# Kernel tuning notes

Hardware: AMD Instinct MI355X
Metric: run time of the kernel (lower is better)

## Reference

```python
import jax, jax.numpy as jnp
import numpy as np

N_GRAPHS = 8
NODES_PER_G = 1024
EDGES_PER_G = 2048
N = N_GRAPHS * NODES_PER_G          # 8192 nodes
E = N_GRAPHS * EDGES_PER_G          # 16384 edges
IN_DIM, EDGE_DIM, HID, OUT_DIM, T = 10, 9, 64, 3, 5
EPS = 1e-6


def _lin(key, fan_in, fan_out):
    kw, kb = jax.random.split(key)
    s = 1.0 / np.sqrt(fan_in)
    return (jax.random.uniform(kw, (fan_in, fan_out), jnp.float32, -s, s),
            jax.random.uniform(kb, (fan_out,), jnp.float32, -s, s))


def setup_inputs() -> dict:
    key = jax.random.key(0)
    ks = jax.random.split(key, 32)
    x = jax.random.normal(ks[0], (N, IN_DIM), jnp.float32)
    edge_attr = jax.random.normal(ks[1], (E, EDGE_DIM), jnp.float32)
    # edges stay within their own graph (block structure)
    src_l = jax.random.randint(ks[2], (E,), 0, NODES_PER_G)
    dst_l = jax.random.randint(ks[3], (E,), 0, NODES_PER_G)
    off = jnp.repeat(jnp.arange(N_GRAPHS, dtype=jnp.int64) * NODES_PER_G, EDGES_PER_G)
    edge_index = jnp.stack([src_l.astype(jnp.int64) + off, dst_l.astype(jnp.int64) + off])
    batch = jnp.repeat(jnp.arange(N_GRAPHS, dtype=jnp.int64), NODES_PER_G)

    lift_w1, lift_b1 = _lin(ks[4], IN_DIM, HID)
    lift_w2, lift_b2 = _lin(ks[5], HID, HID)
    proj_w1, proj_b1 = _lin(ks[6], HID, HID)
    proj_w2, proj_b2 = _lin(ks[7], HID, OUT_DIM)

    def stackp(fn, base):
        ws, bs = zip(*[fn(ks[base + t]) for t in range(T)])
        return jnp.stack(ws), jnp.stack(bs)

    root_w, root_b = stackp(lambda k: _lin(k, HID, HID), 8)
    k_w1, k_b1 = stackp(lambda k: _lin(k, EDGE_DIM, HID), 13)
    k_w2, k_b2 = stackp(lambda k: _lin(k, HID, HID), 18)
    k_w3, k_b3 = stackp(lambda k: _lin(k, HID, HID * HID), 23)

    return dict(x=x, edge_attr=edge_attr,
                lift_w1=lift_w1, lift_b1=lift_b1, lift_w2=lift_w2, lift_b2=lift_b2,
                root_w=root_w, root_b=root_b,
                k_w1=k_w1, k_b1=k_b1, k_w2=k_w2, k_b2=k_b2, k_w3=k_w3, k_b3=k_b3,
                proj_w1=proj_w1, proj_b1=proj_b1, proj_w2=proj_w2, proj_b2=proj_b2,
                edge_index=edge_index, batch=batch)


def reference(x, edge_attr, lift_w1, lift_b1, lift_w2, lift_b2,
              root_w, root_b, k_w1, k_b1, k_w2, k_b2, k_w3, k_b3,
              proj_w1, proj_b1, proj_w2, proj_b2, edge_index, batch):
    src, dst = edge_index[0], edge_index[1]

    # --- per-graph edge_attr standardization (scatter mean/std over each graph's edges) ---
    eb = batch[src]                                           # graph id per edge [E]
    ones_e = jnp.ones((E,), jnp.float32)
    cnt = jax.ops.segment_sum(ones_e, eb, num_segments=N_GRAPHS)          # [G]
    mean = jax.ops.segment_sum(edge_attr, eb, num_segments=N_GRAPHS) / cnt[:, None]
    msq = jax.ops.segment_sum(edge_attr * edge_attr, eb, num_segments=N_GRAPHS) / cnt[:, None]
    std = jnp.sqrt(jnp.clip(msq - mean * mean, 0.0))
    ea = (edge_attr - mean[eb]) / (std[eb] + EPS)             # [E, edge_dim]

    # --- lift MLP ---
    v = jax.nn.relu(x @ lift_w1 + lift_b1) @ lift_w2 + lift_b2  # [N, HID]

    # --- T kernel layers: v' = relu(W_root v + mean_{j->i} K(e_ij) v_j) ---
    deg = jnp.clip(jax.ops.segment_sum(ones_e, dst, num_segments=N), 1.0)  # [N]
    for t in range(T):
        h = jax.nn.relu(ea @ k_w1[t] + k_b1[t])
        h = jax.nn.relu(h @ k_w2[t] + k_b2[t])
        ker = (h @ k_w3[t] + k_b3[t]).reshape(E, HID, HID)    # per-edge 64x64 kernel
        msg = jnp.einsum('eij,ej->ei', ker, v[src])           # [E, HID]
        aggr = jax.ops.segment_sum(msg, dst, num_segments=N) / deg[:, None]
        v = jax.nn.relu(v @ root_w[t] + root_b[t] + aggr)
        # dropout (p=0.1) is identity in eval mode

    # --- project MLP ---
    return jax.nn.relu(v @ proj_w1 + proj_b1) @ proj_w2 + proj_b2  # [N, OUT_DIM]
```

## Files before the change

kernel.cpp:

```cpp
#include <hip/hip_runtime.h>

#define N_GRAPHS    8
#define EDGES_PER_G 2048
#define NN          8192
#define EE          16384
#define IN_DIM      10
#define EDGE_DIM    9
#define HID         64
#define OUT_DIM     3
#define TT          5
#define EPSN        1e-6f

typedef float f32x4 __attribute__((ext_vector_type(4)));
typedef short bf16x8s __attribute__((ext_vector_type(8)));

union BF8 { __bf16 h[8]; bf16x8s v; };

__device__ inline void gl_lds16(const unsigned short* g, unsigned short* l) {
  __builtin_amdgcn_global_load_lds(
      (const __attribute__((address_space(1))) unsigned int*)g,
      (__attribute__((address_space(3))) unsigned int*)l, 16, 0, 0);
}

__device__ inline void edgemlp16(int e0, int tid,
    const float* __restrict__ ear, const float* __restrict__ meanb,
    const float* __restrict__ invstd,
    const float* __restrict__ w1, const float* __restrict__ b1,
    const float* __restrict__ w2, const float* __restrict__ b2,
    float* smem, float* __restrict__ h2T) {
  float (*sh)[68] = (float (*)[68])smem;
  float (*st)[68] = (float (*)[68])(smem + 16 * 68);
  int g = tid >> 6, lane = tid & 63;
  int eb = e0 + g * 4;
  int gg = e0 >> 11;
  const float* mb = meanb + gg * EDGE_DIM;
  const float* is = invstd + gg * EDGE_DIM;
  float xn[4][EDGE_DIM];
#pragma unroll
  for (int k = 0; k < 4; ++k) {
    const float* er = ear + (size_t)(eb + k) * EDGE_DIM;
#pragma unroll
    for (int d = 0; d < EDGE_DIM; ++d) xn[k][d] = (er[d] - mb[d]) * is[d];
  }
  float a0 = b1[lane], a1 = a0, a2 = a0, a3 = a0;
#pragma unroll
  for (int d = 0; d < EDGE_DIM; ++d) {
    float w = w1[d * HID + lane];
    a0 += xn[0][d] * w; a1 += xn[1][d] * w;
    a2 += xn[2][d] * w; a3 += xn[3][d] * w;
  }
  sh[g * 4 + 0][lane] = fmaxf(a0, 0.f);
  sh[g * 4 + 1][lane] = fmaxf(a1, 0.f);
  sh[g * 4 + 2][lane] = fmaxf(a2, 0.f);
  sh[g * 4 + 3][lane] = fmaxf(a3, 0.f);
  __syncthreads();
  float o0 = b2[lane], o1 = o0, o2 = o0, o3 = o0;
#pragma unroll
  for (int h = 0; h < HID; ++h) {
    float w = w2[h * HID + lane];
    o0 += sh[g * 4 + 0][h] * w; o1 += sh[g * 4 + 1][h] * w;
    o2 += sh[g * 4 + 2][h] * w; o3 += sh[g * 4 + 3][h] * w;
  }
  st[g * 4 + 0][lane] = fmaxf(o0, 0.f);
  st[g * 4 + 1][lane] = fmaxf(o1, 0.f);
  st[g * 4 + 2][lane] = fmaxf(o2, 0.f);
  st[g * 4 + 3][lane] = fmaxf(o3, 0.f);
  __syncthreads();
  for (int i = tid; i < HID * 16; i += 256) {
    int c = i >> 4, eo = i & 15;
    h2T[(size_t)c * EE + e0 + eo] = st[eo][c];
  }
}

__global__ __launch_bounds__(256) void k_stats(
    const float* __restrict__ ear, float* __restrict__ meanb,
    float* __restrict__ invstd, float* __restrict__ degf) {
  __shared__ float sw[4][2 * EDGE_DIM];
  int b = blockIdx.x;
  int g = threadIdx.x >> 6, lane = threadIdx.x & 63;
  if (b < N_GRAPHS) {
    int gg = b;
    float ls[EDGE_DIM], lq[EDGE_DIM];
#pragma unroll
    for (int d = 0; d < EDGE_DIM; ++d) { ls[d] = 0.f; lq[d] = 0.f; }
    for (int e = threadIdx.x; e < EDGES_PER_G; e += blockDim.x) {
      const float* row = ear + (size_t)(gg * EDGES_PER_G + e) * EDGE_DIM;
#pragma unroll
      for (int d = 0; d < EDGE_DIM; ++d) { float xv = row[d]; ls[d] += xv; lq[d] += xv * xv; }
    }
#pragma unroll
    for (int d = 0; d < EDGE_DIM; ++d) {
#pragma unroll
      for (int off = 32; off > 0; off >>= 1) {
        ls[d] += __shfl_down(ls[d], off);
        lq[d] += __shfl_down(lq[d], off);
      }
    }
    if (lane == 0) {
#pragma unroll
      for (int d = 0; d < EDGE_DIM; ++d) {
        sw[g][d] = ls[d];
        sw[g][EDGE_DIM + d] = lq[d];
      }
    }
    __syncthreads();
    if (threadIdx.x < EDGE_DIM) {
      int d = threadIdx.x;
      float s0 = sw[0][d] + sw[1][d] + sw[2][d] + sw[3][d];
      float q0 = sw[0][EDGE_DIM + d] + sw[1][EDGE_DIM + d] +
                 sw[2][EDGE_DIM + d] + sw[3][EDGE_DIM + d];
      float m  = s0 * (1.0f / EDGES_PER_G);
      float mq = q0 * (1.0f / EDGES_PER_G);
      float var = fmaxf(mq - m * m, 0.f);
      meanb[gg * EDGE_DIM + d]  = m;
      invstd[gg * EDGE_DIM + d] = 1.f / (sqrtf(var) + EPSN);
    }
  } else {
    int idx = (b - N_GRAPHS) * 256 + threadIdx.x;
    ((float4*)degf)[idx] = make_float4(0.f, 0.f, 0.f, 0.f);
  }
}

#define PRE_EM0   (EE / 16)
#define PRE_LIFT  (NN / 4)
#define PRE_BPREP 1024
#define PRE_DEG   (EE / 256)
#define PRE_ZAG   (NN * HID / 1024)
__global__ __launch_bounds__(256) void k_pre(
    const float* __restrict__ x,
    const float* __restrict__ lw1, const float* __restrict__ lb1,
    const float* __restrict__ lw2, const float* __restrict__ lb2,
    float* __restrict__ v,
    const float* __restrict__ kw3, const float* __restrict__ kb3,
    unsigned short* __restrict__ Bbf,
    const int* __restrict__ dst, float* __restrict__ degf,
    const float* __restrict__ ear, const float* __restrict__ meanb,
    const float* __restrict__ invstd, float* __restrict__ aggr,
    const float* __restrict__ w1, const float* __restrict__ b1,
    const float* __restrict__ w2, const float* __restrict__ b2,
    float* __restrict__ h2T0) {
  __shared__ float smem[2 * 16 * 68];
  int b = blockIdx.x;
  int g = threadIdx.x >> 6, lane = threadIdx.x & 63;
  if (b < PRE_EM0) {
    edgemlp16(b * 16, threadIdx.x, ear, meanb, invstd, w1, b1, w2, b2,
              smem, h2T0);
  } else if (b < PRE_EM0 + PRE_LIFT) {
    float (*sh)[HID] = (float (*)[HID])smem;
    int n = (b - PRE_EM0) * 4 + g;
    const float* xr = x + n * IN_DIM;
    float a = lb1[lane];
#pragma unroll
    for (int d = 0; d < IN_DIM; ++d) a += xr[d] * lw1[d * HID + lane];
    sh[g][lane] = fmaxf(a, 0.f);
    __syncthreads();
    float o = lb2[lane];
#pragma unroll
    for (int h = 0; h < HID; ++h) o += sh[g][h] * lw2[h * HID + lane];
    v[n * HID + lane] = o;
  } else if (b < PRE_EM0 + PRE_LIFT + PRE_BPREP) {
    const int total = TT * 65 * 4096;
    for (int i = (b - (PRE_EM0 + PRE_LIFT)) * 256 + (int)threadIdx.x; i < total;
         i += PRE_BPREP * 256) {
      int xx   = i & 4095;
      int call = i >> 12;
      int t = call / 65;
      int c = call - t * 65;
      int sn = xx >> 9;
      int s  = sn >> 2, nt = sn & 3;
      int l9 = xx & 511;
      int ln = l9 >> 3, jj = l9 & 7;
      int nn15 = ln & 15, qq = ln >> 4;
      int x_in = (nt * 16 + nn15) * 64 + s * 32 + qq * 8 + jj;
      float val = (c < 64) ? kw3[(size_t)(t * 64 + c) * 4096 + x_in]
                           : kb3[(size_t)t * 4096 + x_in];
      union { __bf16 h; unsigned short s16; } u;
      u.h = (__bf16)val;
      Bbf[i] = u.s16;
    }
  } else if (b < PRE_EM0 + PRE_LIFT + PRE_BPREP + PRE_DEG) {
    int e = (b - (PRE_EM0 + PRE_LIFT + PRE_BPREP)) * 256 + threadIdx.x;
    atomicAdd(&degf[dst[e]], 1.f);
  } else {
    int idx = (b - (PRE_EM0 + PRE_LIFT + PRE_BPREP + PRE_DEG)) * 256 + threadIdx.x;
    ((float4*)aggr)[idx] = make_float4(0.f, 0.f, 0.f, 0.f);
  }
}

__global__ __launch_bounds__(256) void k_msg(const float* __restrict__ v,
    const float* __restrict__ h2T_r, const unsigned short* __restrict__ Bt,
    const int* __restrict__ src, const int* __restrict__ dst,
    float* __restrict__ aggr, int nEm,
    const float* __restrict__ ear, const float* __restrict__ meanb,
    const float* __restrict__ invstd,
    const float* __restrict__ w1, const float* __restrict__ b1,
    const float* __restrict__ w2, const float* __restrict__ b2,
    float* __restrict__ h2T_w) {
  __shared__ unsigned short bstage[3][4096];
  int b = blockIdx.x;
  if (b < 1024) {
    int kchunk = b & 3;
    int ebb    = (b >> 2) * 64;
    int w    = threadIdx.x >> 6;
    int lane = threadIdx.x & 63;
    int n15  = lane & 15;
    int q    = lane >> 4;
    int ebase = ebb + w * 16;

    bf16x8s ubf[2];
    {
      int e = ebase + n15;
      const float4* vr = (const float4*)(v + (size_t)src[e] * HID);
      int f0 = q * 2;
#pragma unroll
      for (int s = 0; s < 2; ++s) {
        float4 pa = vr[s * 8 + f0], pb = vr[s * 8 + f0 + 1];
        BF8 u;
        u.h[0] = (__bf16)pa.x; u.h[1] = (__bf16)pa.y;
        u.h[2] = (__bf16)pa.z; u.h[3] = (__bf16)pa.w;
        u.h[4] = (__bf16)pb.x; u.h[5] = (__bf16)pb.y;
        u.h[6] = (__bf16)pb.z; u.h[7] = (__bf16)pb.w;
        ubf[s] = u.v;
      }
    }

    f32x4 acc[4];
#pragma unroll
    for (int nt = 0; nt < 4; ++nt) acc[nt] = (f32x4)0.0f;

    int c0 = kchunk * 16;
    const float* hq = h2T_r + (size_t)c0 * EE + ebase + q * 4;
    const int NCC = (kchunk == 3) ? 17 : 16;

    auto stage = [&](int cc) {
      const unsigned short* gt = (cc < 16)
          ? Bt + (size_t)(c0 + cc) * 4096
          : Bt + (size_t)64 * 4096;
      const unsigned short* gsrc = gt + w * 1024 + lane * 8;
      unsigned short* ldst = &bstage[cc % 3][w * 1024];
      gl_lds16(gsrc, ldst);
      gl_lds16(gsrc + 512, ldst + 512);
    };

    stage(0);
    stage(1);

    for (int cc = 0; cc < NCC; ++cc) {
      asm volatile("s_waitcnt vmcnt(2)" ::: "memory");
      __builtin_amdgcn_s_barrier();
      float4 h4;
      if (cc < 16) h4 = *(const float4*)(hq + (size_t)cc * EE);
      __builtin_amdgcn_sched_barrier(0);
      if (cc + 2 < NCC) stage(cc + 2);
      __builtin_amdgcn_sched_barrier(0);

      const unsigned short* Bs = &bstage[cc % 3][lane * 8];
      bf16x8s bfr[2][4];
#pragma unroll
      for (int s = 0; s < 2; ++s)
#pragma unroll
        for (int nt = 0; nt < 4; ++nt)
          bfr[s][nt] = *(const bf16x8s*)(Bs + (s * 4 + nt) * 512);
      if (cc < 16) {
        f32x4 tmp[4];
#pragma unroll
        for (int nt = 0; nt < 4; ++nt) {
          f32x4 t0 = __builtin_amdgcn_mfma_f32_16x16x32_bf16(
              ubf[0], bfr[0][nt], (f32x4)0.0f, 0, 0, 0);
          tmp[nt] = __builtin_amdgcn_mfma_f32_16x16x32_bf16(
              ubf[1], bfr[1][nt], t0, 0, 0, 0);
        }
#pragma unroll
        for (int nt = 0; nt < 4; ++nt) {
          acc[nt][0] += h4.x * tmp[nt][0];
          acc[nt][1] += h4.y * tmp[nt][1];
          acc[nt][2] += h4.z * tmp[nt][2];
          acc[nt][3] += h4.w * tmp[nt][3];
        }
      } else {
#pragma unroll
        for (int s = 0; s < 2; ++s)
#pragma unroll
          for (int nt = 0; nt < 4; ++nt)
            acc[nt] = __builtin_amdgcn_mfma_f32_16x16x32_bf16(
                ubf[s], bfr[s][nt], acc[nt], 0, 0, 0);
      }
    }

#pragma unroll
    for (int r = 0; r < 4; ++r) {
      int e = ebase + q * 4 + r;
      int d = dst[e];
      float* ag = aggr + (size_t)d * HID;
#pragma unroll
      for (int nt = 0; nt < 4; ++nt)
        atomicAdd(ag + nt * 16 + n15, acc[nt][r]);
    }
  } else if (b < 1024 + nEm) {
    edgemlp16((b - 1024) * 16, threadIdx.x, ear, meanb, invstd,
              w1, b1, w2, b2, (float*)bstage, h2T_w);
  }
}

__global__ __launch_bounds__(256) void k_upd(
    float* __restrict__ v, const float* __restrict__ rw, const float* __restrict__ rb,
    float* __restrict__ aggr, const float* __restrict__ degf) {
  __shared__ float sh[4][HID];
  int g = threadIdx.x >> 6, lane = threadIdx.x & 63;
  int n = blockIdx.x * 4 + g;
  int idx = n * HID + lane;
  sh[g][lane] = v[idx];
  __syncthreads();
  float inv = 1.f / fmaxf(degf[n], 1.f);
  float o = rb[lane] + aggr[idx] * inv;
  aggr[idx] = 0.f;
#pragma unroll
  for (int h = 0; h < HID; ++h) o += sh[g][h] * rw[h * HID + lane];
  v[idx] = fmaxf(o, 0.f);
}

__global__ __launch_bounds__(256) void k_upd_proj(
    const float* __restrict__ v, const float* __restrict__ rw,
    const float* __restrict__ rb,
    const float* __restrict__ aggr, const float* __restrict__ degf,
    const float* __restrict__ pw1, const float* __restrict__ pb1,
    const float* __restrict__ pw2, const float* __restrict__ pb2,
    float* __restrict__ out) {
  __shared__ float sh[4][HID];
  int g = threadIdx.x >> 6, lane = threadIdx.x & 63;
  int n = blockIdx.x * 4 + g;
  int idx = n * HID + lane;
  sh[g][lane] = v[idx];
  __syncthreads();
  float inv = 1.f / fmaxf(degf[n], 1.f);
  float o = rb[lane] + aggr[idx] * inv;
#pragma unroll
  for (int h = 0; h < HID; ++h) o += sh[g][h] * rw[h * HID + lane];
  float vn = fmaxf(o, 0.f);
  __syncthreads();
  sh[g][lane] = vn;
  __syncthreads();
  float a = pb1[lane];
#pragma unroll
  for (int h = 0; h < HID; ++h) a += sh[g][h] * pw1[h * HID + lane];
  float h1 = fmaxf(a, 0.f);
  __syncthreads();
  sh[g][lane] = h1;
  __syncthreads();
  if (lane < OUT_DIM) {
    float oo = pb2[lane];
#pragma unroll
    for (int h = 0; h < HID; ++h) oo += sh[g][h] * pw2[h * OUT_DIM + lane];
    out[n * OUT_DIM + lane] = oo;
  }
}

extern "C" void kernel_launch(void* const* d_in, const int* in_sizes, int n_in,
                              void* d_out, int out_size, void* d_ws, size_t ws_size,
                              hipStream_t stream) {
  const float* x        = (const float*)d_in[0];
  const float* ear      = (const float*)d_in[1];
  const float* lift_w1  = (const float*)d_in[2];
  const float* lift_b1  = (const float*)d_in[3];
  const float* lift_w2  = (const float*)d_in[4];
  const float* lift_b2  = (const float*)d_in[5];
  const float* root_w   = (const float*)d_in[6];
  const float* root_b   = (const float*)d_in[7];
  const float* kw1      = (const float*)d_in[8];
  const float* kb1      = (const float*)d_in[9];
  const float* kw2      = (const float*)d_in[10];
  const float* kb2      = (const float*)d_in[11];
  const float* kw3      = (const float*)d_in[12];
  const float* kb3      = (const float*)d_in[13];
  const float* pw1      = (const float*)d_in[14];
  const float* pb1      = (const float*)d_in[15];
  const float* pw2      = (const float*)d_in[16];
  const float* pb2      = (const float*)d_in[17];
  const int* edge_index = (const int*)d_in[18];
  const int* src = edge_index;
  const int* dst = edge_index + EE;
  float* out = (float*)d_out;

  float* ws     = (float*)d_ws;
  float* aggr   = ws;
  float* degf   = aggr + NN * HID;
  float* h2Ta   = degf + NN;
  float* h2Tb   = h2Ta + (size_t)HID * EE;
  float* vbuf   = h2Tb + (size_t)HID * EE;
  float* meanb  = vbuf + NN * HID;
  float* invstd = meanb + 72;
  unsigned short* Bbf = (unsigned short*)(invstd + 72);

  k_stats<<<2 * N_GRAPHS, 256, 0, stream>>>(ear, meanb, invstd, degf);

  const int PRE_BLOCKS = PRE_EM0 + PRE_LIFT + PRE_BPREP + PRE_DEG + PRE_ZAG;
  k_pre<<<PRE_BLOCKS, 256, 0, stream>>>(
      x, lift_w1, lift_b1, lift_w2, lift_b2, vbuf, kw3, kb3, Bbf,
      dst, degf, ear, meanb, invstd, aggr,
      kw1, kb1, kw2, kb2, h2Ta);

  for (int t = 0; t < TT; ++t) {
    const float* hr = (t & 1) ? h2Tb : h2Ta;
    float*       hw = (t & 1) ? h2Ta : h2Tb;
    int nEm = (t < TT - 1) ? EE / 16 : 0;
    int tt  = (t < TT - 1) ? t + 1 : t;
    k_msg<<<1024 + nEm, 256, 0, stream>>>(
        vbuf, hr, Bbf + (size_t)t * 65 * 4096, src, dst, aggr, nEm,
        ear, meanb, invstd,
        kw1 + (size_t)tt * EDGE_DIM * HID, kb1 + (size_t)tt * HID,
        kw2 + (size_t)tt * HID * HID, kb2 + (size_t)tt * HID, hw);
    if (t < TT - 1) {
      k_upd<<<NN / 4, 256, 0, stream>>>(
          vbuf, root_w + (size_t)t * HID * HID, root_b + (size_t)t * HID,
          aggr, degf);
    } else {
      k_upd_proj<<<NN / 4, 256, 0, stream>>>(
          vbuf, root_w + (size_t)t * HID * HID, root_b + (size_t)t * HID,
          aggr, degf, pw1, pb1, pw2, pb2, out);
    }
  }
}
```

Measured before the change: 334.2 us.

## Replace atomic scatter-add aggregation with CSR gather over per-chunk message buffers

The message kernel no longer atomically adds each edge's partial message into the per-node aggregate. Instead it writes partial messages for each of the four k-chunks to a dense buffer. The update kernel then gathers them per destination node using a CSR built once by a prefix-sum kernel and an edge bucketing kernel. This removes the float atomics and the aggr zeroing, but adds 16 MB of message writes and reads per layer, two setup kernels (one of them a single block), and the edge order within each CSR row depends on atomics.

```diff
diff --git a/kernel.cpp b/kernel.cpp
--- a/kernel.cpp
+++ b/kernel.cpp
@@ -125,7 +125,6 @@
 #define PRE_LIFT  (NN / 4)
 #define PRE_BPREP 1024
 #define PRE_DEG   (EE / 256)
-#define PRE_ZAG   (NN * HID / 1024)
 __global__ __launch_bounds__(256) void k_pre(
     const float* __restrict__ x,
     const float* __restrict__ lw1, const float* __restrict__ lb1,
@@ -135,7 +134,7 @@
     unsigned short* __restrict__ Bbf,
     const int* __restrict__ dst, float* __restrict__ degf,
     const float* __restrict__ ear, const float* __restrict__ meanb,
-    const float* __restrict__ invstd, float* __restrict__ aggr,
+    const float* __restrict__ invstd,
     const float* __restrict__ w1, const float* __restrict__ b1,
     const float* __restrict__ w2, const float* __restrict__ b2,
     float* __restrict__ h2T0) {
@@ -178,19 +177,49 @@
       u.h = (__bf16)val;
       Bbf[i] = u.s16;
     }
-  } else if (b < PRE_EM0 + PRE_LIFT + PRE_BPREP + PRE_DEG) {
+  } else {
     int e = (b - (PRE_EM0 + PRE_LIFT + PRE_BPREP)) * 256 + threadIdx.x;
     atomicAdd(&degf[dst[e]], 1.f);
-  } else {
-    int idx = (b - (PRE_EM0 + PRE_LIFT + PRE_BPREP + PRE_DEG)) * 256 + threadIdx.x;
-    ((float4*)aggr)[idx] = make_float4(0.f, 0.f, 0.f, 0.f);
-  }
+  }
+}
+
+__global__ __launch_bounds__(256) void k_csr1(const float* __restrict__ degf,
+    int* __restrict__ rowptr, int* __restrict__ cur) {
+  __shared__ int ps[256];
+  int tid = threadIdx.x;
+  int base = tid * 32;
+  int loc[32];
+  int s = 0;
+#pragma unroll
+  for (int k = 0; k < 32; ++k) { loc[k] = s; s += (int)degf[base + k]; }
+  ps[tid] = s;
+  __syncthreads();
+  if (tid == 0) {
+    int a = 0;
+    for (int i = 0; i < 256; ++i) { int t = ps[i]; ps[i] = a; a += t; }
+    rowptr[NN] = a;
+  }
+  __syncthreads();
+  int off = ps[tid];
+#pragma unroll
+  for (int k = 0; k < 32; ++k) {
+    rowptr[base + k] = off + loc[k];
+    cur[base + k]    = off + loc[k];
+  }
+}
+
+__global__ __launch_bounds__(256) void k_csr2(const int* __restrict__ dst,
+    int* __restrict__ cur, int* __restrict__ ecsr) {
+  int e = blockIdx.x * 256 + threadIdx.x;
+  int d = dst[e];
+  int pos = atomicAdd(&cur[d], 1);
+  ecsr[pos] = e;
 }
 
 __global__ __launch_bounds__(256) void k_msg(const float* __restrict__ v,
     const float* __restrict__ h2T_r, const unsigned short* __restrict__ Bt,
-    const int* __restrict__ src, const int* __restrict__ dst,
-    float* __restrict__ aggr, int nEm,
+    const int* __restrict__ src,
+    float* __restrict__ msgbuf, int nEm,
     const float* __restrict__ ear, const float* __restrict__ meanb,
     const float* __restrict__ invstd,
     const float* __restrict__ w1, const float* __restrict__ b1,
@@ -287,14 +316,13 @@
       }
     }
 
+    float* mb = msgbuf + (size_t)kchunk * EE * HID;
 #pragma unroll
     for (int r = 0; r < 4; ++r) {
       int e = ebase + q * 4 + r;
-      int d = dst[e];
-      float* ag = aggr + (size_t)d * HID;
 #pragma unroll
       for (int nt = 0; nt < 4; ++nt)
-        atomicAdd(ag + nt * 16 + n15, acc[nt][r]);
+        mb[(size_t)e * HID + nt * 16 + n15] = acc[nt][r];
     }
   } else if (b < 1024 + nEm) {
     edgemlp16((b - 1024) * 16, threadIdx.x, ear, meanb, invstd,
@@ -304,16 +332,25 @@
 
 __global__ __launch_bounds__(256) void k_upd(
     float* __restrict__ v, const float* __restrict__ rw, const float* __restrict__ rb,
-    float* __restrict__ aggr, const float* __restrict__ degf) {
+    const float* __restrict__ msgbuf, const float* __restrict__ degf,
+    const int* __restrict__ rowptr, const int* __restrict__ ecsr) {
   __shared__ float sh[4][HID];
   int g = threadIdx.x >> 6, lane = threadIdx.x & 63;
   int n = blockIdx.x * 4 + g;
   int idx = n * HID + lane;
   sh[g][lane] = v[idx];
   __syncthreads();
+  int r0 = rowptr[n], r1 = rowptr[n + 1];
+  float s = 0.f;
+  for (int j = r0; j < r1; ++j) {
+    int e = ecsr[j];
+    s += msgbuf[(size_t)e * HID + lane]
+       + msgbuf[((size_t)EE + e) * HID + lane]
+       + msgbuf[((size_t)2 * EE + e) * HID + lane]
+       + msgbuf[((size_t)3 * EE + e) * HID + lane];
+  }
   float inv = 1.f / fmaxf(degf[n], 1.f);
-  float o = rb[lane] + aggr[idx] * inv;
-  aggr[idx] = 0.f;
+  float o = rb[lane] + s * inv;
 #pragma unroll
   for (int h = 0; h < HID; ++h) o += sh[g][h] * rw[h * HID + lane];
   v[idx] = fmaxf(o, 0.f);
@@ -322,7 +359,8 @@
 __global__ __launch_bounds__(256) void k_upd_proj(
     const float* __restrict__ v, const float* __restrict__ rw,
     const float* __restrict__ rb,
-    const float* __restrict__ aggr, const float* __restrict__ degf,
+    const float* __restrict__ msgbuf, const float* __restrict__ degf,
+    const int* __restrict__ rowptr, const int* __restrict__ ecsr,
     const float* __restrict__ pw1, const float* __restrict__ pb1,
     const float* __restrict__ pw2, const float* __restrict__ pb2,
     float* __restrict__ out) {
@@ -332,8 +370,17 @@
   int idx = n * HID + lane;
   sh[g][lane] = v[idx];
   __syncthreads();
+  int r0 = rowptr[n], r1 = rowptr[n + 1];
+  float s = 0.f;
+  for (int j = r0; j < r1; ++j) {
+    int e = ecsr[j];
+    s += msgbuf[(size_t)e * HID + lane]
+       + msgbuf[((size_t)EE + e) * HID + lane]
+       + msgbuf[((size_t)2 * EE + e) * HID + lane]
+       + msgbuf[((size_t)3 * EE + e) * HID + lane];
+  }
   float inv = 1.f / fmaxf(degf[n], 1.f);
-  float o = rb[lane] + aggr[idx] * inv;
+  float o = rb[lane] + s * inv;
 #pragma unroll
   for (int h = 0; h < HID; ++h) o += sh[g][h] * rw[h * HID + lane];
   float vn = fmaxf(o, 0.f);
@@ -382,22 +429,28 @@
   float* out = (float*)d_out;
 
   float* ws     = (float*)d_ws;
-  float* aggr   = ws;
-  float* degf   = aggr + NN * HID;
+  float* msgbuf = ws;
+  float* degf   = msgbuf + (size_t)4 * EE * HID;
   float* h2Ta   = degf + NN;
   float* h2Tb   = h2Ta + (size_t)HID * EE;
   float* vbuf   = h2Tb + (size_t)HID * EE;
   float* meanb  = vbuf + NN * HID;
   float* invstd = meanb + 72;
   unsigned short* Bbf = (unsigned short*)(invstd + 72);
+  int* rowptr = (int*)(Bbf + (size_t)TT * 65 * 4096);
+  int* cur    = rowptr + NN + 1;
+  int* ecsr   = cur + NN;
 
   k_stats<<<2 * N_GRAPHS, 256, 0, stream>>>(ear, meanb, invstd, degf);
 
-  const int PRE_BLOCKS = PRE_EM0 + PRE_LIFT + PRE_BPREP + PRE_DEG + PRE_ZAG;
+  const int PRE_BLOCKS = PRE_EM0 + PRE_LIFT + PRE_BPREP + PRE_DEG;
   k_pre<<<PRE_BLOCKS, 256, 0, stream>>>(
       x, lift_w1, lift_b1, lift_w2, lift_b2, vbuf, kw3, kb3, Bbf,
-      dst, degf, ear, meanb, invstd, aggr,
+      dst, degf, ear, meanb, invstd,
       kw1, kb1, kw2, kb2, h2Ta);
+
+  k_csr1<<<1, 256, 0, stream>>>(degf, rowptr, cur);
+  k_csr2<<<EE / 256, 256, 0, stream>>>(dst, cur, ecsr);
 
   for (int t = 0; t < TT; ++t) {
     const float* hr = (t & 1) ? h2Tb : h2Ta;
@@ -405,18 +458,18 @@
     int nEm = (t < TT - 1) ? EE / 16 : 0;
     int tt  = (t < TT - 1) ? t + 1 : t;
     k_msg<<<1024 + nEm, 256, 0, stream>>>(
-        vbuf, hr, Bbf + (size_t)t * 65 * 4096, src, dst, aggr, nEm,
+        vbuf, hr, Bbf + (size_t)t * 65 * 4096, src, msgbuf, nEm,
         ear, meanb, invstd,
         kw1 + (size_t)tt * EDGE_DIM * HID, kb1 + (size_t)tt * HID,
         kw2 + (size_t)tt * HID * HID, kb2 + (size_t)tt * HID, hw);
     if (t < TT - 1) {
       k_upd<<<NN / 4, 256, 0, stream>>>(
           vbuf, root_w + (size_t)t * HID * HID, root_b + (size_t)t * HID,
-          aggr, degf);
+          msgbuf, degf, rowptr, ecsr);
     } else {
       k_upd_proj<<<NN / 4, 256, 0, stream>>>(
           vbuf, root_w + (size_t)t * HID * HID, root_b + (size_t)t * HID,
-          aggr, degf, pw1, pb1, pw2, pb2, out);
-    }
-  }
-}
+          msgbuf, degf, rowptr, ecsr, pw1, pb1, pw2, pb2, out);
+    }
+  }
+}
```

Result: faster. 325.1 us (median of 3 runs) (-2.7%).
